# Kernel tuning notes

Hardware: AMD Instinct MI355X
Metric: run time of the kernel (lower is better)

## Reference

```python
import jax, jax.numpy as jnp
import numpy as np

BLOCK = 512
WINDOW = 2
NEG = -1e9


def _pad_to_block(x, block):
    pad_len = (-x.shape[1]) % block
    if pad_len:
        x = jnp.pad(x, ((0, 0), (0, pad_len), (0, 0)))
    return x


def setup_inputs() -> dict:
    key = jax.random.key(0)
    ks = jax.random.split(key, 8)
    B, Lq, Lk, C = 2, 8192, 8192, 128
    s = 1.0 / np.sqrt(C)
    return {
        "query": jax.random.normal(ks[0], (B, Lq, C), jnp.float32),
        "key_value": jax.random.normal(ks[1], (B, Lk, C), jnp.float32),
        "Wq": jax.random.normal(ks[2], (C, C), jnp.float32) * s,
        "bq": jax.random.normal(ks[3], (C,), jnp.float32) * 0.01,
        "Wkv": jax.random.normal(ks[4], (C, 2 * C), jnp.float32) * s,
        "bkv": jax.random.normal(ks[5], (2 * C,), jnp.float32) * 0.01,
        "Wo": jax.random.normal(ks[6], (C, C), jnp.float32) * s,
        "bo": jax.random.normal(ks[7], (C,), jnp.float32) * 0.01,
    }


def reference(query, key_value, Wq, bq, Wkv, bkv, Wo, bo):
    B, Lq, C = query.shape
    qp = _pad_to_block(query, BLOCK)
    kp = _pad_to_block(key_value, BLOCK)
    q = qp @ Wq + bq                      # [B, Lq_pad, C]
    kv = kp @ Wkv + bkv                   # [B, Lk_pad, 2C]
    k, v = kv[..., :C], kv[..., C:]
    nq = qp.shape[1] // BLOCK
    nk = kp.shape[1] // BLOCK
    qb = q.reshape(B, nq, BLOCK, C)
    kb = k.reshape(B, nk, BLOCK, C)
    vb = v.reshape(B, nk, BLOCK, C)
    allowed = jnp.abs(jnp.arange(nq)[:, None] - jnp.arange(nk)[None, :]) <= WINDOW  # [nq, nk]
    # scores: [B, nq, nk, s, d] with s = q-pos in block, d = k-pos in block
    scores = jnp.einsum('bqsc,bkdc->bqksd', qb, kb) / jnp.sqrt(jnp.asarray(C, qb.dtype))
    scores = jnp.where(allowed[None, :, :, None, None], scores, NEG)
    # NOTE: faithful to original torch code, softmax over axis=3 (the 's' axis)
    attn = jax.nn.softmax(scores, axis=3)
    out = jnp.einsum('bqksd,bkdc->bqsc', attn, vb)
    out = out.reshape(B, nq * BLOCK, C)[:, :Lq]
    return out @ Wo + bo
```

## Files before the change

kernel.cpp:

```cpp
#include <hip/hip_runtime.h>

typedef _Float16 f16;
typedef _Float16 half8 __attribute__((ext_vector_type(8)));
typedef float floatx4 __attribute__((ext_vector_type(4)));

#define MFMA16(a,b,c) __builtin_amdgcn_mfma_f32_16x16x32_f16((a),(b),(c),0,0,0)
#define RSL2E 0.12751743f

__device__ __forceinline__ void split2(float x, f16 &h, f16 &l) {
  f16 hh = (f16)x;
  h = hh;
  l = (f16)(x - (float)hh);
}

__device__ __forceinline__ void stage_rows64(const f16* __restrict__ g, int gstride,
                                             f16* lds, int rows, int tid, int nthr) {
  int total = rows * 8;
  for (int idx = tid; idx < total; idx += nthr) {
    int row = idx >> 3, slot = idx & 7;
    float4 v = *(const float4*)(g + (size_t)row * gstride + slot * 8);
    int lofs = ((row << 7) + (slot << 4)) ^ ((row & 7) << 4);
    *(float4*)((char*)lds + lofs) = v;
  }
}
__device__ __forceinline__ void stage_rows128(const f16* __restrict__ g, int gstride,
                                              f16* lds, int rows, int tid, int nthr) {
  int total = rows * 16;
  for (int idx = tid; idx < total; idx += nthr) {
    int row = idx >> 4, slot = idx & 15;
    float4 v = *(const float4*)(g + (size_t)row * gstride + slot * 8);
    int lofs = ((row << 8) + (slot << 4)) ^ ((row & 7) << 4);
    *(float4*)((char*)lds + lofs) = v;
  }
}
__device__ __forceinline__ void stage_split64(const float* __restrict__ g, int gstride,
                                              f16* ldsh, f16* ldsl, int rows,
                                              int tid, int nthr) {
  int total = rows * 16;
  for (int idx = tid; idx < total; idx += nthr) {
    int row = idx >> 4, cg = idx & 15;
    float4 va = *(const float4*)(g + (size_t)row * gstride + cg * 4);
    union { f16 a[4]; uint2 u; } hh, ll;
    split2(va.x, hh.a[0], ll.a[0]);
    split2(va.y, hh.a[1], ll.a[1]);
    split2(va.z, hh.a[2], ll.a[2]);
    split2(va.w, hh.a[3], ll.a[3]);
    int lofs = ((row << 7) + (cg << 3)) ^ ((row & 7) << 4);
    *(uint2*)((char*)ldsh + lofs) = hh.u;
    *(uint2*)((char*)ldsl + lofs) = ll.u;
  }
}
__device__ __forceinline__ half8 fragP128(const f16* lds, int row, int kofs) {
  int ofs = ((row << 7) + (kofs << 1)) ^ ((row & 7) << 4);
  return *(const half8*)((const char*)lds + ofs);
}
__device__ __forceinline__ half8 fragP256(const f16* lds, int row, int kofs) {
  int ofs = ((row << 8) + (kofs << 1)) ^ ((row & 7) << 4);
  return *(const half8*)((const char*)lds + ofs);
}

__global__ void k_splitW(const float* __restrict__ Wq, const float* __restrict__ Wkv,
                         const float* __restrict__ Wo,
                         f16* WqTh, f16* WqTl, f16* WkvTh, f16* WkvTl,
                         f16* WoTh, f16* WoTl) {
  int idx = blockIdx.x * 256 + threadIdx.x;
  if (idx >= 65536) return;
  float v; f16 *ph, *pl; int dst;
  if (idx < 16384) {
    int n = idx >> 7, c = idx & 127;
    v = Wq[c * 128 + n]; ph = WqTh; pl = WqTl; dst = idx;
  } else if (idx < 49152) {
    int t = idx - 16384; int n = t >> 7, c = t & 127;
    v = Wkv[c * 256 + n]; ph = WkvTh; pl = WkvTl; dst = t;
  } else {
    int t = idx - 49152; int n = t >> 7, c = t & 127;
    v = Wo[c * 128 + n]; ph = WoTh; pl = WoTl; dst = t;
  }
  f16 h, l; split2(v, h, l);
  ph[dst] = h; pl[dst] = l;
}

__global__ __launch_bounds__(512, 2)
void k_proj(const float* __restrict__ query, const float* __restrict__ key_value,
            const f16* __restrict__ WqTh, const f16* __restrict__ WqTl,
            const f16* __restrict__ WkvTh, const f16* __restrict__ WkvTl,
            const float* __restrict__ bq, const float* __restrict__ bkv,
            f16* __restrict__ qhp, f16* __restrict__ khp, f16* __restrict__ vT) {
  int pidx = blockIdx.x >> 8, blk = blockIdx.x & 255;
  const float* A; const f16 *BTh, *BTl; const float* bias; f16* out; int mode;
  if (pidx == 0)      { A = query;     BTh = WqTh;          BTl = WqTl;          bias = bq;        out = qhp; mode = 0; }
  else if (pidx == 1) { A = key_value; BTh = WkvTh;         BTl = WkvTl;         bias = bkv;       out = khp; mode = 0; }
  else                { A = key_value; BTh = WkvTh + 16384; BTl = WkvTl + 16384; bias = bkv + 128; out = vT;  mode = 1; }
  __shared__ f16 pool[24576];
  f16* sAh = pool;
  f16* sAl = pool + 4096;
  f16* sBh = pool + 8192;
  f16* sBl = pool + 16384;
  int tid = threadIdx.x, wave = tid >> 6, lane = tid & 63, lg = lane >> 4, lr = lane & 15;
  int wm = wave >> 2, wn = wave & 3;
  size_t rowbase = (size_t)blk * 64;
  floatx4 zero = {0.f, 0.f, 0.f, 0.f};
  floatx4 acc[2][2] = {{zero, zero}, {zero, zero}};
  for (int cc = 0; cc < 128; cc += 64) {
    __syncthreads();
    stage_split64(A + rowbase * 128 + cc, 128, sAh, sAl, 64, tid, 512);
    stage_rows64(BTh + cc, 128, sBh, 128, tid, 512);
    stage_rows64(BTl + cc, 128, sBl, 128, tid, 512);
    __syncthreads();
    for (int kc = 0; kc < 64; kc += 32) {
      half8 ah[2], al[2];
      for (int fm = 0; fm < 2; fm++) {
        ah[fm] = fragP128(sAh, wm * 32 + fm * 16 + lr, kc + lg * 8);
        al[fm] = fragP128(sAl, wm * 32 + fm * 16 + lr, kc + lg * 8);
      }
      for (int fn = 0; fn < 2; fn++) {
        half8 bh = fragP128(sBh, wn * 32 + fn * 16 + lr, kc + lg * 8);
        half8 bl = fragP128(sBl, wn * 32 + fn * 16 + lr, kc + lg * 8);
        for (int fm = 0; fm < 2; fm++) {
          acc[fm][fn] = MFMA16(ah[fm], bh, acc[fm][fn]);
          acc[fm][fn] = MFMA16(ah[fm], bl, acc[fm][fn]);
          acc[fm][fn] = MFMA16(al[fm], bh, acc[fm][fn]);
        }
      }
    }
  }
  __syncthreads();
  f16* e = pool;
  for (int fm = 0; fm < 2; fm++) for (int fn = 0; fn < 2; fn++) {
    int n = wn * 32 + fn * 16 + lr;
    float bs = bias[n];
    for (int jj = 0; jj < 4; jj++) {
      int m = wm * 32 + fm * 16 + lg * 4 + jj;
      e[m * 136 + n] = (f16)(acc[fm][fn][jj] + bs);
    }
  }
  __syncthreads();
  if (mode == 0) {
    for (int idx = tid; idx < 1024; idx += 512) {
      int r = idx >> 4, sl = idx & 15;
      *(float4*)(out + (rowbase + r) * 128 + sl * 8) =
          *(const float4*)((const char*)e + r * 272 + sl * 16);
    }
  } else {
    size_t bidx = rowbase >> 13, lofs = rowbase & 8191;
    for (int idx = tid; idx < 1024; idx += 512) {
      int c = idx >> 3, sl = idx & 7;
      union { f16 a[8]; float4 v; } th;
      for (int t = 0; t < 8; t++) th.a[t] = e[(sl * 8 + t) * 136 + c];
      *(float4*)(out + (bidx * 128 + c) * 8192 + lofs + sl * 8) = th.v;
    }
  }
}

__global__ __launch_bounds__(512, 2)
void k_final(const float* __restrict__ Pbuf, const float* __restrict__ U,
             const f16* __restrict__ BTh, const f16* __restrict__ BTl,
             const float* __restrict__ bias, float* __restrict__ out) {
  __shared__ f16 pool[24576];
  f16* sAh = pool;
  f16* sAl = pool + 4096;
  f16* sBh = pool + 8192;
  f16* sBl = pool + 16384;
  int tid = threadIdx.x, wave = tid >> 6, lane = tid & 63, lg = lane >> 4, lr = lane & 15;
  int wm = wave >> 2, wn = wave & 3;
  size_t rowbase = (size_t)blockIdx.x * 64;
  int b = (int)(rowbase >> 13), r0 = (int)(rowbase & 8191);
  int i = r0 >> 9, st = (r0 >> 6) & 7;
  const float* p0 = Pbuf + ((size_t)(((b * 16 + i) * 8 + st) * 4)) * 8192;
  const float* p1 = p0 + 8192;
  const float* p2 = p0 + 16384;
  const float* p3 = p0 + 24576;
  const float* Ub = U + ((size_t)b * 16 + i) * 128;
  floatx4 zero = {0.f, 0.f, 0.f, 0.f};
  floatx4 acc[2][2] = {{zero, zero}, {zero, zero}};
  for (int cc = 0; cc < 128; cc += 64) {
    __syncthreads();
    for (int idx = tid; idx < 1024; idx += 512) {
      int row = idx >> 4, cg = idx & 15;
      int c = cc + cg * 4;
      float4 a0 = *(const float4*)(p0 + row * 128 + c);
      float4 a1 = *(const float4*)(p1 + row * 128 + c);
      float4 a2 = *(const float4*)(p2 + row * 128 + c);
      float4 a3 = *(const float4*)(p3 + row * 128 + c);
      float4 uu = *(const float4*)(Ub + c);
      float vals[4] = {(a0.x + a1.x) + (a2.x + a3.x) + uu.x,
                       (a0.y + a1.y) + (a2.y + a3.y) + uu.y,
                       (a0.z + a1.z) + (a2.z + a3.z) + uu.z,
                       (a0.w + a1.w) + (a2.w + a3.w) + uu.w};
      union { f16 a[4]; uint2 u; } hh, ll;
      for (int t = 0; t < 4; t++) split2(vals[t], hh.a[t], ll.a[t]);
      int lofs = ((row << 7) + (cg << 3)) ^ ((row & 7) << 4);
      *(uint2*)((char*)sAh + lofs) = hh.u;
      *(uint2*)((char*)sAl + lofs) = ll.u;
    }
    stage_rows64(BTh + cc, 128, sBh, 128, tid, 512);
    stage_rows64(BTl + cc, 128, sBl, 128, tid, 512);
    __syncthreads();
    for (int kc = 0; kc < 64; kc += 32) {
      half8 ah[2], al[2];
      for (int fm = 0; fm < 2; fm++) {
        ah[fm] = fragP128(sAh, wm * 32 + fm * 16 + lr, kc + lg * 8);
        al[fm] = fragP128(sAl, wm * 32 + fm * 16 + lr, kc + lg * 8);
      }
      for (int fn = 0; fn < 2; fn++) {
        half8 bh = fragP128(sBh, wn * 32 + fn * 16 + lr, kc + lg * 8);
        half8 bl = fragP128(sBl, wn * 32 + fn * 16 + lr, kc + lg * 8);
        for (int fm = 0; fm < 2; fm++) {
          acc[fm][fn] = MFMA16(ah[fm], bh, acc[fm][fn]);
          acc[fm][fn] = MFMA16(ah[fm], bl, acc[fm][fn]);
          acc[fm][fn] = MFMA16(al[fm], bh, acc[fm][fn]);
        }
      }
    }
  }
  __syncthreads();
  float* ef = (float*)pool;
  for (int fm = 0; fm < 2; fm++) for (int fn = 0; fn < 2; fn++) {
    int n = wn * 32 + fn * 16 + lr;
    float bs = bias[n];
    for (int jj = 0; jj < 4; jj++) {
      int m = wm * 32 + fm * 16 + lg * 4 + jj;
      ef[m * 132 + n] = acc[fm][fn][jj] + bs;
    }
  }
  __syncthreads();
  for (int idx = tid; idx < 2048; idx += 512) {
    int r = idx >> 5, sl = idx & 31;
    *(float4*)(out + (rowbase + r) * 128 + sl * 4) = *(const float4*)(ef + r * 132 + sl * 4);
  }
}

__global__ void k_U(const f16* __restrict__ vT, float* __restrict__ U) {
  int b = blockIdx.x >> 7, c = blockIdx.x & 127;
  int tid = threadIdx.x;
  const f16* r = vT + ((size_t)b * 128 + c) * 8192;
  float s = 0.f;
  const float4* r4 = (const float4*)(r + tid * 32);
  for (int t = 0; t < 4; t++) {
    float4 v = r4[t];
    const f16* a = (const f16*)&v;
    for (int u = 0; u < 8; u++) s += (float)a[u];
  }
  __shared__ float part[256];
  __shared__ float bs[16];
  part[tid] = s;
  __syncthreads();
  if (tid < 16) {
    float t = 0.f;
    for (int u = 0; u < 16; u++) t += part[tid * 16 + u];
    bs[tid] = t;
  }
  __syncthreads();
  if (tid < 16) {
    int i = tid;
    float tot = 0.f;
    for (int j = 0; j < 16; j++) tot += bs[j];
    int j0 = i - 2 < 0 ? 0 : i - 2;
    int j1 = i + 2 > 15 ? 15 : i + 2;
    float win = 0.f;
    for (int j = j0; j <= j1; j++) win += bs[j];
    U[((size_t)b * 16 + i) * 128 + c] = (tot - win) * (1.0f / 512.0f);
  }
}

__global__ __launch_bounds__(512, 4)
void k_passA(const f16* __restrict__ kp, const f16* __restrict__ qp,
             float* __restrict__ Z) {
  int bid = blockIdx.x;
  int wg = (bid & 7) * 80 + (bid >> 3);
  int dchunk = wg & 3; int rest = wg >> 2;
  int slot = rest % 5; int rest2 = rest / 5;
  int i = rest2 & 15; int b = rest2 >> 4;
  int j = i - 2 + slot;
  if (j < 0 || j > 15) return;
  __shared__ f16 sK[16384], sQ[16384];
  int tid = threadIdx.x, wave = tid >> 6, lane = tid & 63, lg = lane >> 4, lr = lane & 15;
  int wm = wave >> 1, wn = wave & 1;
  size_t krow = (size_t)b * 8192 + j * 512 + dchunk * 128;
  stage_rows128(kp + krow * 128, 128, sK, 128, tid, 512);
  float zp[2][4] = {{0.f,0.f,0.f,0.f},{0.f,0.f,0.f,0.f}};
  floatx4 zero = {0.f, 0.f, 0.f, 0.f};
  for (int sc = 0; sc < 4; sc++) {
    __syncthreads();
    size_t qrow = (size_t)b * 8192 + i * 512 + sc * 128;
    stage_rows128(qp + qrow * 128, 128, sQ, 128, tid, 512);
    __syncthreads();
    floatx4 acc[2][4] = {{zero,zero,zero,zero},{zero,zero,zero,zero}};
    for (int kc = 0; kc < 128; kc += 32) {
      half8 ah[2];
      for (int fm = 0; fm < 2; fm++)
        ah[fm] = fragP256(sK, wm * 32 + fm * 16 + lr, kc + lg * 8);
      for (int fn = 0; fn < 4; fn++) {
        half8 bh = fragP256(sQ, wn * 64 + fn * 16 + lr, kc + lg * 8);
        for (int fm = 0; fm < 2; fm++)
          acc[fm][fn] = MFMA16(ah[fm], bh, acc[fm][fn]);
      }
    }
    for (int fm = 0; fm < 2; fm++) for (int fn = 0; fn < 4; fn++)
      for (int jj = 0; jj < 4; jj++)
        zp[fm][jj] += exp2f(acc[fm][fn][jj] * RSL2E);
  }
  for (int off = 1; off < 16; off <<= 1)
    for (int fm = 0; fm < 2; fm++) for (int jj = 0; jj < 4; jj++)
      zp[fm][jj] += __shfl_xor(zp[fm][jj], off, 64);
  __syncthreads();
  float* sred = (float*)sQ;
  if (lr == 0) {
    for (int fm = 0; fm < 2; fm++) for (int jj = 0; jj < 4; jj++) {
      int d = wm * 32 + fm * 16 + lg * 4 + jj;
      sred[wn * 128 + d] = zp[fm][jj];
    }
  }
  __syncthreads();
  if (tid < 128) {
    size_t zb = (((size_t)(b * 16 + i) * 16 + j) * 512) + dchunk * 128;
    Z[zb + tid] = sred[tid] + sred[128 + tid];
  }
}

__global__ __launch_bounds__(512, 4)
void k_passB(const f16* __restrict__ qp, const f16* __restrict__ kp,
             const f16* __restrict__ vT,
             const float* __restrict__ Z, float* __restrict__ Pbuf) {
  int bid = blockIdx.x;
  int wg = ((bid & 7) << 7) | (bid >> 3);
  int dq = wg & 3, st = (wg >> 2) & 7, i = (wg >> 5) & 15, b = wg >> 9;
  __shared__ __align__(16) char pool[40960];
  f16* sQ  = (f16*)pool;
  f16* sKV = (f16*)(pool + 16384);
  f16* sE  = (f16*)(pool + 32768);
  int tid = threadIdx.x, wave = tid >> 6, lane = tid & 63, lg = lane >> 4, lr = lane & 15;
  int w1m = wave >> 1, w1n = wave & 1;
  int w2m = wave >> 2, w2n = wave & 3;
  int krr = tid >> 3, ksl = tid & 7;
  int lofsA = ((krr << 7) + (ksl << 4)) ^ ((krr & 7) << 4);
  int lofsB = (((krr + 64) << 7) + (ksl << 4)) ^ ((krr & 7) << 4);
  int myVdsub = (wave < 4) ? 1 : 0;
  int tt = (wave >= 4) ? (tid - 256) : tid;
  int vr0 = tt >> 3, vsl = tt & 7;
  int vlofs[4];
  #pragma unroll
  for (int t = 0; t < 4; t++)
    vlofs[t] = (((vr0 + 32 * t) << 7) + (vsl << 4)) ^ ((vr0 & 7) << 4);
  size_t qrow = (size_t)b * 8192 + i * 512 + st * 64;
  stage_rows128(qp + qrow * 128, 128, sQ, 64, tid, 512);
  floatx4 zero = {0.f, 0.f, 0.f, 0.f};
  floatx4 acc2[2][2] = {{zero, zero}, {zero, zero}};
  const f16* vbase = vT + (size_t)b * 1048576;
  for (int slot = 0; slot < 5; slot++) {
    int j = i - 2 + slot;
    if (j < 0 || j > 15) continue;
    {
      int dchunk = dq;
      const f16* kb = kp + ((size_t)b * 8192 + j * 512 + dchunk * 128) * 128;
      float4 p0a = *(const float4*)(kb + krr * 128 + ksl * 8);
      float4 p0b = *(const float4*)(kb + (krr + 64) * 128 + ksl * 8);
      const f16* gv = vbase + (size_t)j * 512 + dchunk * 128 + myVdsub * 64;
      float4 vr_0 = *(const float4*)(gv + (size_t)vr0 * 8192 + vsl * 8);
      float4 vr_1 = *(const float4*)(gv + (size_t)(vr0 + 32) * 8192 + vsl * 8);
      float4 vr_2 = *(const float4*)(gv + (size_t)(vr0 + 64) * 8192 + vsl * 8);
      float4 vr_3 = *(const float4*)(gv + (size_t)(vr0 + 96) * 8192 + vsl * 8);
      float rz[2][4];
      {
        size_t zb = (((size_t)(b * 16 + i) * 16 + j) * 512) + dchunk * 128;
        #pragma unroll
        for (int fm = 0; fm < 2; fm++)
          #pragma unroll
          for (int jj = 0; jj < 4; jj++)
            rz[fm][jj] = 1.0f / Z[zb + w1m * 32 + fm * 16 + lg * 4 + jj];
      }
      floatx4 acc1[2][2] = {{zero, zero}, {zero, zero}};
      __syncthreads();
      *(float4*)((char*)sKV + lofsA) = p0a;
      *(float4*)((char*)sKV + lofsB) = p0b;
      float4 p1a = *(const float4*)(kb + krr * 128 + 64 + ksl * 8);
      float4 p1b = *(const float4*)(kb + (krr + 64) * 128 + 64 + ksl * 8);
      __syncthreads();
      for (int kc = 0; kc < 64; kc += 32) {
        half8 ah[2];
        for (int fm = 0; fm < 2; fm++)
          ah[fm] = fragP128(sKV, w1m * 32 + fm * 16 + lr, kc + lg * 8);
        for (int fn = 0; fn < 2; fn++) {
          half8 bh = fragP256(sQ, w1n * 32 + fn * 16 + lr, kc + lg * 8);
          for (int fm = 0; fm < 2; fm++)
            acc1[fm][fn] = MFMA16(ah[fm], bh, acc1[fm][fn]);
        }
      }
      __syncthreads();
      *(float4*)((char*)sKV + lofsA) = p1a;
      *(float4*)((char*)sKV + lofsB) = p1b;
      __syncthreads();
      for (int kc = 0; kc < 64; kc += 32) {
        half8 ah[2];
        for (int fm = 0; fm < 2; fm++)
          ah[fm] = fragP128(sKV, w1m * 32 + fm * 16 + lr, kc + lg * 8);
        for (int fn = 0; fn < 2; fn++) {
          half8 bh = fragP256(sQ, w1n * 32 + fn * 16 + lr, 64 + kc + lg * 8);
          for (int fm = 0; fm < 2; fm++)
            acc1[fm][fn] = MFMA16(ah[fm], bh, acc1[fm][fn]);
        }
      }
      for (int dsub = 0; dsub < 2; dsub++) {
        __syncthreads();
        if ((wave >> 2) == dsub) {
          #pragma unroll
          for (int fm = 0; fm < 2; fm++)
            #pragma unroll
            for (int fn = 0; fn < 2; fn++) {
              int s = w1n * 32 + fn * 16 + lr;
              int ds0 = (w1m & 1) * 32 + fm * 16 + lg * 4;
              union { f16 a[4]; float2 u; } pk;
              #pragma unroll
              for (int jj = 0; jj < 4; jj++)
                pk.a[jj] = (f16)(exp2f(acc1[fm][fn][jj] * RSL2E) * rz[fm][jj]);
              int ofs = ((s << 7) + (ds0 << 1)) ^ ((s & 7) << 4);
              *(float2*)((char*)sE + ofs) = pk.u;
            }
        } else {
          *(float4*)((char*)sKV + vlofs[0]) = vr_0;
          *(float4*)((char*)sKV + vlofs[1]) = vr_1;
          *(float4*)((char*)sKV + vlofs[2]) = vr_2;
          *(float4*)((char*)sKV + vlofs[3]) = vr_3;
        }
        __syncthreads();
        for (int kc = 0; kc < 64; kc += 32) {
          half8 ah[2];
          for (int fm = 0; fm < 2; fm++)
            ah[fm] = fragP128(sE, w2m * 32 + fm * 16 + lr, kc + lg * 8);
          for (int fn = 0; fn < 2; fn++) {
            half8 bh = fragP128(sKV, w2n * 32 + fn * 16 + lr, kc + lg * 8);
            for (int fm = 0; fm < 2; fm++)
              acc2[fm][fn] = MFMA16(ah[fm], bh, acc2[fm][fn]);
          }
        }
      }
    }
  }
  __syncthreads();
  float* ef = (float*)pool;
  for (int fm = 0; fm < 2; fm++) for (int fn = 0; fn < 2; fn++) {
    int c = w2n * 32 + fn * 16 + lr;
    for (int jj = 0; jj < 4; jj++) {
      int s = w2m * 32 + fm * 16 + lg * 4 + jj;
      ef[s * 128 + c] = acc2[fm][fn][jj];
    }
  }
  __syncthreads();
  float* po = Pbuf + ((size_t)((((b * 16 + i) * 8 + st) * 4) + dq)) * 8192;
  for (int idx = tid; idx < 2048; idx += 512)
    ((float4*)po)[idx] = ((const float4*)ef)[idx];
}

extern "C" void kernel_launch(void* const* d_in, const int* in_sizes, int n_in,
                              void* d_out, int out_size, void* d_ws, size_t ws_size,
                              hipStream_t stream) {
  const float* query     = (const float*)d_in[0];
  const float* key_value = (const float*)d_in[1];
  const float* Wq  = (const float*)d_in[2];
  const float* bq  = (const float*)d_in[3];
  const float* Wkv = (const float*)d_in[4];
  const float* bkv = (const float*)d_in[5];
  const float* Wo  = (const float*)d_in[6];
  const float* bo  = (const float*)d_in[7];
  float* out = (float*)d_out;

  char* ws = (char*)d_ws;
  size_t off = 0;
  auto alloc = [&](size_t bytes) -> char* {
    char* p = ws + off;
    off += (bytes + 255) & ~(size_t)255;
    return p;
  };
  const size_t SZH = (size_t)16384 * 128 * 2;
  f16* qhp  = (f16*)alloc(SZH);
  f16* khp  = (f16*)alloc(SZH);
  f16* vT   = (f16*)alloc(SZH);
  float* Pbuf = (float*)alloc((size_t)1024 * 8192 * 4);
  f16* WqTh  = (f16*)alloc(32768); f16* WqTl  = (f16*)alloc(32768);
  f16* WkvTh = (f16*)alloc(65536); f16* WkvTl = (f16*)alloc(65536);
  f16* WoTh  = (f16*)alloc(32768); f16* WoTl  = (f16*)alloc(32768);
  float* Zb = (float*)alloc((size_t)2 * 16 * 16 * 512 * 4);
  float* Ub = (float*)alloc((size_t)2 * 16 * 128 * 4);
  if (off > ws_size) return;

  k_splitW<<<256, 256, 0, stream>>>(Wq, Wkv, Wo, WqTh, WqTl, WkvTh, WkvTl, WoTh, WoTl);
  k_proj<<<768, 512, 0, stream>>>(query, key_value, WqTh, WqTl, WkvTh, WkvTl,
                                  bq, bkv, qhp, khp, vT);
  k_U<<<256, 256, 0, stream>>>(vT, Ub);
  k_passA<<<640, 512, 0, stream>>>(khp, qhp, Zb);
  k_passB<<<1024, 512, 0, stream>>>(qhp, khp, vT, Zb, Pbuf);
  k_final<<<256, 512, 0, stream>>>(Pbuf, Ub, WoTh, WoTl, bo, out);
}
```

Before: 113.4 us.

## Stage full 128-wide K and V tiles in LDS to cut barriers in passB

```diff
diff --git a/kernel.cpp b/kernel.cpp
--- a/kernel.cpp
+++ b/kernel.cpp
@@ -325,23 +325,18 @@
   int bid = blockIdx.x;
   int wg = ((bid & 7) << 7) | (bid >> 3);
   int dq = wg & 3, st = (wg >> 2) & 7, i = (wg >> 5) & 15, b = wg >> 9;
-  __shared__ __align__(16) char pool[40960];
+  __shared__ __align__(16) char pool[65536];
   f16* sQ  = (f16*)pool;
   f16* sKV = (f16*)(pool + 16384);
-  f16* sE  = (f16*)(pool + 32768);
+  f16* sE  = (f16*)(pool + 49152);
   int tid = threadIdx.x, wave = tid >> 6, lane = tid & 63, lg = lane >> 4, lr = lane & 15;
   int w1m = wave >> 1, w1n = wave & 1;
   int w2m = wave >> 2, w2n = wave & 3;
-  int krr = tid >> 3, ksl = tid & 7;
-  int lofsA = ((krr << 7) + (ksl << 4)) ^ ((krr & 7) << 4);
-  int lofsB = (((krr + 64) << 7) + (ksl << 4)) ^ ((krr & 7) << 4);
-  int myVdsub = (wave < 4) ? 1 : 0;
-  int tt = (wave >= 4) ? (tid - 256) : tid;
-  int vr0 = tt >> 3, vsl = tt & 7;
-  int vlofs[4];
-  #pragma unroll
-  for (int t = 0; t < 4; t++)
-    vlofs[t] = (((vr0 + 32 * t) << 7) + (vsl << 4)) ^ ((vr0 & 7) << 4);
+  int srow = tid >> 4, sslot = tid & 15;
+  int sl0 = (((srow      ) << 8) + (sslot << 4)) ^ ((srow & 7) << 4);
+  int sl1 = (((srow +  32) << 8) + (sslot << 4)) ^ ((srow & 7) << 4);
+  int sl2 = (((srow +  64) << 8) + (sslot << 4)) ^ ((srow & 7) << 4);
+  int sl3 = (((srow +  96) << 8) + (sslot << 4)) ^ ((srow & 7) << 4);
   size_t qrow = (size_t)b * 8192 + i * 512 + st * 64;
   stage_rows128(qp + qrow * 128, 128, sQ, 64, tid, 512);
   floatx4 zero = {0.f, 0.f, 0.f, 0.f};
@@ -350,89 +345,71 @@
   for (int slot = 0; slot < 5; slot++) {
     int j = i - 2 + slot;
     if (j < 0 || j > 15) continue;
+    const f16* kb = kp + ((size_t)b * 8192 + j * 512 + dq * 128) * 128;
+    float4 k0 = *(const float4*)(kb + (size_t)(srow      ) * 128 + sslot * 8);
+    float4 k1 = *(const float4*)(kb + (size_t)(srow +  32) * 128 + sslot * 8);
+    float4 k2 = *(const float4*)(kb + (size_t)(srow +  64) * 128 + sslot * 8);
+    float4 k3 = *(const float4*)(kb + (size_t)(srow +  96) * 128 + sslot * 8);
+    const f16* gv = vbase + (size_t)j * 512 + dq * 128;
+    float4 v0 = *(const float4*)(gv + (size_t)(srow      ) * 8192 + sslot * 8);
+    float4 v1 = *(const float4*)(gv + (size_t)(srow +  32) * 8192 + sslot * 8);
+    float4 v2 = *(const float4*)(gv + (size_t)(srow +  64) * 8192 + sslot * 8);
+    float4 v3 = *(const float4*)(gv + (size_t)(srow +  96) * 8192 + sslot * 8);
+    float rz[2][4];
     {
-      int dchunk = dq;
-      const f16* kb = kp + ((size_t)b * 8192 + j * 512 + dchunk * 128) * 128;
-      float4 p0a = *(const float4*)(kb + krr * 128 + ksl * 8);
-      float4 p0b = *(const float4*)(kb + (krr + 64) * 128 + ksl * 8);
-      const f16* gv = vbase + (size_t)j * 512 + dchunk * 128 + myVdsub * 64;
-      float4 vr_0 = *(const float4*)(gv + (size_t)vr0 * 8192 + vsl * 8);
-      float4 vr_1 = *(const float4*)(gv + (size_t)(vr0 + 32) * 8192 + vsl * 8);
-      float4 vr_2 = *(const float4*)(gv + (size_t)(vr0 + 64) * 8192 + vsl * 8);
-      float4 vr_3 = *(const float4*)(gv + (size_t)(vr0 + 96) * 8192 + vsl * 8);
-      float rz[2][4];
-      {
-        size_t zb = (((size_t)(b * 16 + i) * 16 + j) * 512) + dchunk * 128;
+      size_t zb = (((size_t)(b * 16 + i) * 16 + j) * 512) + dq * 128;
+      #pragma unroll
+      for (int fm = 0; fm < 2; fm++)
         #pragma unroll
-        for (int fm = 0; fm < 2; fm++)
-          #pragma unroll
-          for (int jj = 0; jj < 4; jj++)
-            rz[fm][jj] = 1.0f / Z[zb + w1m * 32 + fm * 16 + lg * 4 + jj];
-      }
-      floatx4 acc1[2][2] = {{zero, zero}, {zero, zero}};
-      __syncthreads();
-      *(float4*)((char*)sKV + lofsA) = p0a;
-      *(float4*)((char*)sKV + lofsB) = p0b;
-      float4 p1a = *(const float4*)(kb + krr * 128 + 64 + ksl * 8);
-      float4 p1b = *(const float4*)(kb + (krr + 64) * 128 + 64 + ksl * 8);
-      __syncthreads();
-      for (int kc = 0; kc < 64; kc += 32) {
-        half8 ah[2];
-        for (int fm = 0; fm < 2; fm++)
-          ah[fm] = fragP128(sKV, w1m * 32 + fm * 16 + lr, kc + lg * 8);
-        for (int fn = 0; fn < 2; fn++) {
-          half8 bh = fragP256(sQ, w1n * 32 + fn * 16 + lr, kc + lg * 8);
-          for (int fm = 0; fm < 2; fm++)
-            acc1[fm][fn] = MFMA16(ah[fm], bh, acc1[fm][fn]);
-        }
-      }
-      __syncthreads();
-      *(float4*)((char*)sKV + lofsA) = p1a;
-      *(float4*)((char*)sKV + lofsB) = p1b;
-      __syncthreads();
-      for (int kc = 0; kc < 64; kc += 32) {
-        half8 ah[2];
-        for (int fm = 0; fm < 2; fm++)
-          ah[fm] = fragP128(sKV, w1m * 32 + fm * 16 + lr, kc + lg * 8);
-        for (int fn = 0; fn < 2; fn++) {
-          half8 bh = fragP256(sQ, w1n * 32 + fn * 16 + lr, 64 + kc + lg * 8);
-          for (int fm = 0; fm < 2; fm++)
-            acc1[fm][fn] = MFMA16(ah[fm], bh, acc1[fm][fn]);
-        }
-      }
-      for (int dsub = 0; dsub < 2; dsub++) {
-        __syncthreads();
-        if ((wave >> 2) == dsub) {
-          #pragma unroll
-          for (int fm = 0; fm < 2; fm++)
-            #pragma unroll
-            for (int fn = 0; fn < 2; fn++) {
-              int s = w1n * 32 + fn * 16 + lr;
-              int ds0 = (w1m & 1) * 32 + fm * 16 + lg * 4;
-              union { f16 a[4]; float2 u; } pk;
-              #pragma unroll
-              for (int jj = 0; jj < 4; jj++)
-                pk.a[jj] = (f16)(exp2f(acc1[fm][fn][jj] * RSL2E) * rz[fm][jj]);
-              int ofs = ((s << 7) + (ds0 << 1)) ^ ((s & 7) << 4);
-              *(float2*)((char*)sE + ofs) = pk.u;
-            }
-        } else {
-          *(float4*)((char*)sKV + vlofs[0]) = vr_0;
-          *(float4*)((char*)sKV + vlofs[1]) = vr_1;
-          *(float4*)((char*)sKV + vlofs[2]) = vr_2;
-          *(float4*)((char*)sKV + vlofs[3]) = vr_3;
-        }
-        __syncthreads();
-        for (int kc = 0; kc < 64; kc += 32) {
-          half8 ah[2];
-          for (int fm = 0; fm < 2; fm++)
-            ah[fm] = fragP128(sE, w2m * 32 + fm * 16 + lr, kc + lg * 8);
-          for (int fn = 0; fn < 2; fn++) {
-            half8 bh = fragP128(sKV, w2n * 32 + fn * 16 + lr, kc + lg * 8);
-            for (int fm = 0; fm < 2; fm++)
-              acc2[fm][fn] = MFMA16(ah[fm], bh, acc2[fm][fn]);
-          }
-        }
+        for (int jj = 0; jj < 4; jj++)
+          rz[fm][jj] = 1.0f / Z[zb + w1m * 32 + fm * 16 + lg * 4 + jj];
+    }
+    __syncthreads();
+    *(float4*)((char*)sKV + sl0) = k0;
+    *(float4*)((char*)sKV + sl1) = k1;
+    *(float4*)((char*)sKV + sl2) = k2;
+    *(float4*)((char*)sKV + sl3) = k3;
+    __syncthreads();
+    floatx4 acc1[2][2] = {{zero, zero}, {zero, zero}};
+    #pragma unroll
+    for (int kc = 0; kc < 128; kc += 32) {
+      half8 ah0 = fragP256(sKV, w1m * 32 + lr, kc + lg * 8);
+      half8 ah1 = fragP256(sKV, w1m * 32 + 16 + lr, kc + lg * 8);
+      #pragma unroll
+      for (int fn = 0; fn < 2; fn++) {
+        half8 bq = fragP256(sQ, w1n * 32 + fn * 16 + lr, kc + lg * 8);
+        acc1[0][fn] = MFMA16(ah0, bq, acc1[0][fn]);
+        acc1[1][fn] = MFMA16(ah1, bq, acc1[1][fn]);
+      }
+    }
+    __syncthreads();
+    #pragma unroll
+    for (int fm = 0; fm < 2; fm++)
+      #pragma unroll
+      for (int fn = 0; fn < 2; fn++) {
+        int s = w1n * 32 + fn * 16 + lr;
+        int d0 = w1m * 32 + fm * 16 + lg * 4;
+        union { f16 a[4]; float2 u; } pk;
+        #pragma unroll
+        for (int jj = 0; jj < 4; jj++)
+          pk.a[jj] = (f16)(exp2f(acc1[fm][fn][jj] * RSL2E) * rz[fm][jj]);
+        int ofs = ((s << 8) + (d0 << 1)) ^ ((s & 7) << 4);
+        *(float2*)((char*)sE + ofs) = pk.u;
+      }
+    *(float4*)((char*)sKV + sl0) = v0;
+    *(float4*)((char*)sKV + sl1) = v1;
+    *(float4*)((char*)sKV + sl2) = v2;
+    *(float4*)((char*)sKV + sl3) = v3;
+    __syncthreads();
+    #pragma unroll
+    for (int kc = 0; kc < 128; kc += 32) {
+      half8 ea0 = fragP256(sE, w2m * 32 + lr, kc + lg * 8);
+      half8 ea1 = fragP256(sE, w2m * 32 + 16 + lr, kc + lg * 8);
+      #pragma unroll
+      for (int fn = 0; fn < 2; fn++) {
+        half8 bh = fragP256(sKV, w2n * 32 + fn * 16 + lr, kc + lg * 8);
+        acc2[0][fn] = MFMA16(ea0, bh, acc2[0][fn]);
+        acc2[1][fn] = MFMA16(ea1, bh, acc2[1][fn]);
       }
     }
   }
```

Measured after the change: 112.3 us. About the same (-0.9%).
